# Kernel tuning notes

Measured on AMD Instinct MI355X. Metric: run time of the kernel, lower is better.

The kernel has to match this reference:

```python
import jax, jax.numpy as jnp
import numpy as np

N, K, M, DIM = 131072, 16, 128, 64


def setup_inputs() -> dict:
    key = jax.random.key(0)
    kx, ks, ka, kb = jax.random.split(key, 4)
    return {
        "x": jax.random.normal(kx, (N, DIM), dtype=jnp.float32),
        "s": jax.random.normal(ks, (K,), dtype=jnp.float32),
        "a": jax.random.normal(ka, (K, M, DIM), dtype=jnp.float32),
        "b": jax.random.normal(kb, (K, M), dtype=jnp.float32),
    }


def reference(x, s, a, b):
    # scores[k, n, m] = x[n, :] @ a[k, m, :] + b[k, m]  (batched GEMM over k)
    scores = jnp.einsum("nd,kmd->knm", x, a) + b[:, None, :]
    # per-expert logsumexp over the m affine pieces -> [k, n]
    lse = jax.nn.logsumexp(scores, axis=-1)
    # signed sum over experts -> [n]
    return jnp.einsum("k,kn->n", s, lse)
```

## Files before the change

### kernel.cpp

```cpp
#include <hip/hip_runtime.h>
#include <hip/hip_bf16.h>

#define NROWS 131072
#define KEXP 16
#define MPC 128
#define DIMD 64

typedef float f32x4  __attribute__((ext_vector_type(4)));
typedef float f32x16 __attribute__((ext_vector_type(16)));
typedef short s16x8  __attribute__((ext_vector_type(8)));

#define L2E 1.4426950408889634f
#define LN2 0.6931471805599453f

static __device__ inline unsigned int b2u(__hip_bfloat162 h) {
    union { __hip_bfloat162 h; unsigned int u; } c;
    c.h = h;
    return c.u;
}

static __device__ inline int4 cvt8s(float4 f0, float4 f1, float sc) {
    __hip_bfloat162 p0 = __float22bfloat162_rn(make_float2(f0.x * sc, f0.y * sc));
    __hip_bfloat162 p1 = __float22bfloat162_rn(make_float2(f0.z * sc, f0.w * sc));
    __hip_bfloat162 p2 = __float22bfloat162_rn(make_float2(f1.x * sc, f1.y * sc));
    __hip_bfloat162 p3 = __float22bfloat162_rn(make_float2(f1.z * sc, f1.w * sc));
    int4 pk;
    pk.x = (int)b2u(p0); pk.y = (int)b2u(p1); pk.z = (int)b2u(p2); pk.w = (int)b2u(p3);
    return pk;
}

static __device__ inline void async_copy16(const void* g, void* l) {
    __builtin_amdgcn_global_load_lds(
        (const __attribute__((address_space(1))) unsigned int*)g,
        (__attribute__((address_space(3))) unsigned int*)l, 16, 0, 0);
}

__global__ void prep_kernel(const float* __restrict__ a, const float* __restrict__ b,
                            short* __restrict__ abff) {
    const int u   = blockIdx.x * 256 + threadIdx.x;
    const int k   = u / 1280;
    const int rem = u - k * 1280;
    const int mt  = rem / 320;
    const int rc  = rem - mt * 320;
    const int c   = rc >> 6;
    const int ul  = rc & 63;
    int4 pk;
    if (c < 4) {
        const float* p = a + (size_t)(k * MPC + mt * 32 + (ul & 31)) * DIMD
                           + c * 16 + (ul >> 5) * 8;
        pk = cvt8s(*(const float4*)(p), *(const float4*)(p + 4), L2E);
    } else {
        pk.x = 0; pk.y = 0; pk.z = 0; pk.w = 0;
        if (ul < 32) {
            union { __hip_bfloat16 h; unsigned short us; } cv;
            cv.h = __float2bfloat16(b[k * MPC + mt * 32 + ul] * L2E);
            pk.x = (int)cv.us;
        }
    }
    *(int4*)(abff + (size_t)u * 8) = pk;
}

__global__ __launch_bounds__(256, 4)
void fused_kernel(const float* __restrict__ x, const float* __restrict__ s,
                  const short* __restrict__ abff, float* __restrict__ out) {
    __shared__ int4 abuf[2][1280];

    const int tid  = threadIdx.x;
    const int w    = tid >> 6;
    const int l    = tid & 63;
    const int ln   = l & 31;
    const int half = l >> 5;

    const int family = blockIdx.x & 1;
    const int r0w    = (blockIdx.x >> 1) * 256 + w * 64;

    union { int4 i; s16x8 v; } Bf[2][4];
#pragma unroll
    for (int nt = 0; nt < 2; ++nt)
#pragma unroll
        for (int c = 0; c < 4; ++c) {
            const float* gp = x + (size_t)(r0w + nt * 32 + ln) * DIMD + c * 16 + half * 8;
            float4 f0 = *(const float4*)(gp);
            float4 f1 = *(const float4*)(gp + 4);
            Bf[nt][c].i = cvt8s(f0, f1, 1.0f);
        }

    union { int4 i; s16x8 v; } Bones;
    Bones.i.x = (half == 0) ? 0x3F80 : 0;
    Bones.i.y = 0; Bones.i.z = 0; Bones.i.w = 0;

    {
        const short* src = abff + (size_t)(family * 8) * 10240;
#pragma unroll
        for (int i = 0; i < 5; ++i) {
            const int ch = w * 5 + i;
            async_copy16(src + ch * 512 + l * 8, (char*)&abuf[0][0] + ch * 1024);
        }
    }
    __syncthreads();

    float racc0 = 0.f, racc1 = 0.f;

    for (int k = 0; k < 8; ++k) {
        const int kf = family * 8 + k;
        const int kb = k & 1;

        if (k + 1 < 8) {
            const short* src = abff + (size_t)(kf + 1) * 10240;
#pragma unroll
            for (int i = 0; i < 5; ++i) {
                const int ch = w * 5 + i;
                async_copy16(src + ch * 512 + l * 8,
                             (char*)&abuf[kb ^ 1][0] + ch * 1024);
            }
        }

        const float sk2 = s[kf] * LN2;
        float esum0 = 0.f, esum1 = 0.f;

#pragma unroll
        for (int mt = 0; mt < 4; ++mt) {
            s16x8 Af[5];
#pragma unroll
            for (int c = 0; c < 5; ++c)
                Af[c] = *(const s16x8*)((const short*)&abuf[kb][0] + (mt * 5 + c) * 512 + l * 8);

            {
                f32x16 acc = {};
#pragma unroll
                for (int c = 0; c < 4; ++c)
                    acc = __builtin_amdgcn_mfma_f32_32x32x16_bf16(Af[c], Bf[0][c].v, acc, 0, 0, 0);
                acc = __builtin_amdgcn_mfma_f32_32x32x16_bf16(Af[4], Bones.v, acc, 0, 0, 0);
                float s0 = 0.f, s1 = 0.f, s2 = 0.f, s3 = 0.f;
#pragma unroll
                for (int r = 0; r < 4; ++r) {
                    s0 += __builtin_amdgcn_exp2f(acc[4 * r + 0]);
                    s1 += __builtin_amdgcn_exp2f(acc[4 * r + 1]);
                    s2 += __builtin_amdgcn_exp2f(acc[4 * r + 2]);
                    s3 += __builtin_amdgcn_exp2f(acc[4 * r + 3]);
                }
                esum0 += (s0 + s1) + (s2 + s3);
            }
            {
                f32x16 acc = {};
#pragma unroll
                for (int c = 0; c < 4; ++c)
                    acc = __builtin_amdgcn_mfma_f32_32x32x16_bf16(Af[c], Bf[1][c].v, acc, 0, 0, 0);
                acc = __builtin_amdgcn_mfma_f32_32x32x16_bf16(Af[4], Bones.v, acc, 0, 0, 0);
                float s0 = 0.f, s1 = 0.f, s2 = 0.f, s3 = 0.f;
#pragma unroll
                for (int r = 0; r < 4; ++r) {
                    s0 += __builtin_amdgcn_exp2f(acc[4 * r + 0]);
                    s1 += __builtin_amdgcn_exp2f(acc[4 * r + 1]);
                    s2 += __builtin_amdgcn_exp2f(acc[4 * r + 2]);
                    s3 += __builtin_amdgcn_exp2f(acc[4 * r + 3]);
                }
                esum1 += (s0 + s1) + (s2 + s3);
            }
        }

        float tot0 = esum0 + __shfl_xor(esum0, 32);
        float tot1 = esum1 + __shfl_xor(esum1, 32);
        racc0 = fmaf(sk2, __log2f(tot0), racc0);
        racc1 = fmaf(sk2, __log2f(tot1), racc1);

        __syncthreads();
    }

    atomicAdd(&out[r0w + half * 32 + ln], half ? racc1 : racc0);
}

extern "C" void kernel_launch(void* const* d_in, const int* in_sizes, int n_in,
                              void* d_out, int out_size, void* d_ws, size_t ws_size,
                              hipStream_t stream) {
    const float* x = (const float*)d_in[0];
    const float* s = (const float*)d_in[1];
    const float* a = (const float*)d_in[2];
    const float* b = (const float*)d_in[3];
    float* out = (float*)d_out;

    short* abff = (short*)d_ws;

    hipMemsetAsync(d_out, 0, (size_t)NROWS * sizeof(float), stream);
    prep_kernel<<<80, 256, 0, stream>>>(a, b, abff);
    fused_kernel<<<NROWS / 128, 256, 0, stream>>>(x, s, abff, out);
}
```

Measured before the change: 121.7 us.

## Split experts four ways per block, halve LDS stages, fold output zeroing into prep

Each row tile is now covered by four blocks, each handling 4 experts instead of two blocks handling 8. The grid doubles, and the per-expert weight tile is streamed in half-tiles through a smaller double-buffered LDS, which halves shared memory per block and allows 8 blocks per CU. The output memset is dropped and the zeroing moved into the prep kernel, saving one launch. The costs are that x is loaded and converted twice as often, atomics on the output double, and there are more barriers per expert.

Result: slower. 353.3 us (+190.3%).

```diff
diff --git a/kernel.cpp b/kernel.cpp
--- a/kernel.cpp
+++ b/kernel.cpp
@@ -36,7 +36,7 @@
 }
 
 __global__ void prep_kernel(const float* __restrict__ a, const float* __restrict__ b,
-                            short* __restrict__ abff) {
+                            short* __restrict__ abff, float* __restrict__ out) {
     const int u   = blockIdx.x * 256 + threadIdx.x;
     const int k   = u / 1280;
     const int rem = u - k * 1280;
@@ -58,12 +58,14 @@
         }
     }
     *(int4*)(abff + (size_t)u * 8) = pk;
-}
-
-__global__ __launch_bounds__(256, 4)
+
+    for (int i = u; i < NROWS; i += 80 * 256) out[i] = 0.f;
+}
+
+__global__ __launch_bounds__(256, 8)
 void fused_kernel(const float* __restrict__ x, const float* __restrict__ s,
                   const short* __restrict__ abff, float* __restrict__ out) {
-    __shared__ int4 abuf[2][1280];
+    __shared__ int4 abuf[2][640];
 
     const int tid  = threadIdx.x;
     const int w    = tid >> 6;
@@ -71,8 +73,8 @@
     const int ln   = l & 31;
     const int half = l >> 5;
 
-    const int family = blockIdx.x & 1;
-    const int r0w    = (blockIdx.x >> 1) * 256 + w * 64;
+    const int family = blockIdx.x & 3;
+    const int r0w    = (blockIdx.x >> 2) * 256 + w * 64;
 
     union { int4 i; s16x8 v; } Bf[2][4];
 #pragma unroll
@@ -89,82 +91,94 @@
     Bones.i.x = (half == 0) ? 0x3F80 : 0;
     Bones.i.y = 0; Bones.i.z = 0; Bones.i.w = 0;
 
+    const int kf0 = family * 4;
+
     {
-        const short* src = abff + (size_t)(family * 8) * 10240;
-#pragma unroll
-        for (int i = 0; i < 5; ++i) {
-            const int ch = w * 5 + i;
-            async_copy16(src + ch * 512 + l * 8, (char*)&abuf[0][0] + ch * 1024);
+        const short* src = abff + (size_t)kf0 * 10240;
+#pragma unroll
+        for (int i = 0; i < 3; ++i) {
+            const int ch = w + 4 * i;
+            if (ch < 10)
+                async_copy16(src + ch * 512 + l * 8, (char*)&abuf[0][0] + ch * 1024);
         }
     }
     __syncthreads();
 
     float racc0 = 0.f, racc1 = 0.f;
 
-    for (int k = 0; k < 8; ++k) {
-        const int kf = family * 8 + k;
-        const int kb = k & 1;
-
-        if (k + 1 < 8) {
-            const short* src = abff + (size_t)(kf + 1) * 10240;
-#pragma unroll
-            for (int i = 0; i < 5; ++i) {
-                const int ch = w * 5 + i;
-                async_copy16(src + ch * 512 + l * 8,
-                             (char*)&abuf[kb ^ 1][0] + ch * 1024);
-            }
-        }
-
+#pragma unroll
+    for (int k = 0; k < 4; ++k) {
+        const int kf  = kf0 + k;
         const float sk2 = s[kf] * LN2;
         float esum0 = 0.f, esum1 = 0.f;
 
 #pragma unroll
-        for (int mt = 0; mt < 4; ++mt) {
-            s16x8 Af[5];
-#pragma unroll
-            for (int c = 0; c < 5; ++c)
-                Af[c] = *(const s16x8*)((const short*)&abuf[kb][0] + (mt * 5 + c) * 512 + l * 8);
-
-            {
-                f32x16 acc = {};
-#pragma unroll
-                for (int c = 0; c < 4; ++c)
-                    acc = __builtin_amdgcn_mfma_f32_32x32x16_bf16(Af[c], Bf[0][c].v, acc, 0, 0, 0);
-                acc = __builtin_amdgcn_mfma_f32_32x32x16_bf16(Af[4], Bones.v, acc, 0, 0, 0);
-                float s0 = 0.f, s1 = 0.f, s2 = 0.f, s3 = 0.f;
-#pragma unroll
-                for (int r = 0; r < 4; ++r) {
-                    s0 += __builtin_amdgcn_exp2f(acc[4 * r + 0]);
-                    s1 += __builtin_amdgcn_exp2f(acc[4 * r + 1]);
-                    s2 += __builtin_amdgcn_exp2f(acc[4 * r + 2]);
-                    s3 += __builtin_amdgcn_exp2f(acc[4 * r + 3]);
+        for (int h = 0; h < 2; ++h) {
+            const int g   = k * 2 + h;
+            const int buf = g & 1;
+
+            if (g < 7) {
+                const int gn = g + 1;
+                const short* src = abff + (size_t)(kf0 + (gn >> 1)) * 10240
+                                        + (size_t)(gn & 1) * 5120;
+#pragma unroll
+                for (int i = 0; i < 3; ++i) {
+                    const int ch = w + 4 * i;
+                    if (ch < 10)
+                        async_copy16(src + ch * 512 + l * 8,
+                                     (char*)&abuf[buf ^ 1][0] + ch * 1024);
                 }
-                esum0 += (s0 + s1) + (s2 + s3);
             }
-            {
-                f32x16 acc = {};
-#pragma unroll
-                for (int c = 0; c < 4; ++c)
-                    acc = __builtin_amdgcn_mfma_f32_32x32x16_bf16(Af[c], Bf[1][c].v, acc, 0, 0, 0);
-                acc = __builtin_amdgcn_mfma_f32_32x32x16_bf16(Af[4], Bones.v, acc, 0, 0, 0);
-                float s0 = 0.f, s1 = 0.f, s2 = 0.f, s3 = 0.f;
-#pragma unroll
-                for (int r = 0; r < 4; ++r) {
-                    s0 += __builtin_amdgcn_exp2f(acc[4 * r + 0]);
-                    s1 += __builtin_amdgcn_exp2f(acc[4 * r + 1]);
-                    s2 += __builtin_amdgcn_exp2f(acc[4 * r + 2]);
-                    s3 += __builtin_amdgcn_exp2f(acc[4 * r + 3]);
+
+#pragma unroll
+            for (int mtl = 0; mtl < 2; ++mtl) {
+                s16x8 Af[5];
+#pragma unroll
+                for (int c = 0; c < 5; ++c)
+                    Af[c] = *(const s16x8*)((const short*)&abuf[buf][0]
+                                            + (mtl * 5 + c) * 512 + l * 8);
+
+                {
+                    f32x16 acc = {};
+#pragma unroll
+                    for (int c = 0; c < 4; ++c)
+                        acc = __builtin_amdgcn_mfma_f32_32x32x16_bf16(Af[c], Bf[0][c].v, acc, 0, 0, 0);
+                    acc = __builtin_amdgcn_mfma_f32_32x32x16_bf16(Af[4], Bones.v, acc, 0, 0, 0);
+                    float s0 = 0.f, s1 = 0.f, s2 = 0.f, s3 = 0.f;
+#pragma unroll
+                    for (int r = 0; r < 4; ++r) {
+                        s0 += __builtin_amdgcn_exp2f(acc[4 * r + 0]);
+                        s1 += __builtin_amdgcn_exp2f(acc[4 * r + 1]);
+                        s2 += __builtin_amdgcn_exp2f(acc[4 * r + 2]);
+                        s3 += __builtin_amdgcn_exp2f(acc[4 * r + 3]);
+                    }
+                    esum0 += (s0 + s1) + (s2 + s3);
                 }
-                esum1 += (s0 + s1) + (s2 + s3);
+                {
+                    f32x16 acc = {};
+#pragma unroll
+                    for (int c = 0; c < 4; ++c)
+                        acc = __builtin_amdgcn_mfma_f32_32x32x16_bf16(Af[c], Bf[1][c].v, acc, 0, 0, 0);
+                    acc = __builtin_amdgcn_mfma_f32_32x32x16_bf16(Af[4], Bones.v, acc, 0, 0, 0);
+                    float s0 = 0.f, s1 = 0.f, s2 = 0.f, s3 = 0.f;
+#pragma unroll
+                    for (int r = 0; r < 4; ++r) {
+                        s0 += __builtin_amdgcn_exp2f(acc[4 * r + 0]);
+                        s1 += __builtin_amdgcn_exp2f(acc[4 * r + 1]);
+                        s2 += __builtin_amdgcn_exp2f(acc[4 * r + 2]);
+                        s3 += __builtin_amdgcn_exp2f(acc[4 * r + 3]);
+                    }
+                    esum1 += (s0 + s1) + (s2 + s3);
+                }
             }
+
+            __syncthreads();
         }
 
         float tot0 = esum0 + __shfl_xor(esum0, 32);
         float tot1 = esum1 + __shfl_xor(esum1, 32);
         racc0 = fmaf(sk2, __log2f(tot0), racc0);
         racc1 = fmaf(sk2, __log2f(tot1), racc1);
-
-        __syncthreads();
     }
 
     atomicAdd(&out[r0w + half * 32 + ln], half ? racc1 : racc0);
@@ -181,7 +195,6 @@
 
     short* abff = (short*)d_ws;
 
-    hipMemsetAsync(d_out, 0, (size_t)NROWS * sizeof(float), stream);
-    prep_kernel<<<80, 256, 0, stream>>>(a, b, abff);
-    fused_kernel<<<NROWS / 128, 256, 0, stream>>>(x, s, abff, out);
-}
+    prep_kernel<<<80, 256, 0, stream>>>(a, b, abff, out);
+    fused_kernel<<<NROWS / 64, 256, 0, stream>>>(x, s, abff, out);
+}
```

## Fold weight conversion into main kernel and drop prep, memset and LDS staging

Applied to the files above, without the earlier changes.

Removes the separate prep kernel and output memset. Each wave now reads the fp32 expert weights straight from global memory, converts them to bf16 in registers and runs all 16 experts for 32 rows. The output is stored directly instead of added atomically. This cuts two launches, the atomics and the LDS double buffering, but every wave now repeats the global loads and bf16 conversion of a for every row tile, which adds VALU and L2 traffic inside the inner loop.

Result: slower. 302.9 us (+148.9%).

```diff
diff --git a/kernel.cpp b/kernel.cpp
--- a/kernel.cpp
+++ b/kernel.cpp
@@ -6,7 +6,6 @@
 #define MPC 128
 #define DIMD 64
 
-typedef float f32x4  __attribute__((ext_vector_type(4)));
 typedef float f32x16 __attribute__((ext_vector_type(16)));
 typedef short s16x8  __attribute__((ext_vector_type(8)));
 
@@ -29,145 +28,76 @@
     return pk;
 }
 
-static __device__ inline void async_copy16(const void* g, void* l) {
-    __builtin_amdgcn_global_load_lds(
-        (const __attribute__((address_space(1))) unsigned int*)g,
-        (__attribute__((address_space(3))) unsigned int*)l, 16, 0, 0);
-}
-
-__global__ void prep_kernel(const float* __restrict__ a, const float* __restrict__ b,
-                            short* __restrict__ abff) {
-    const int u   = blockIdx.x * 256 + threadIdx.x;
-    const int k   = u / 1280;
-    const int rem = u - k * 1280;
-    const int mt  = rem / 320;
-    const int rc  = rem - mt * 320;
-    const int c   = rc >> 6;
-    const int ul  = rc & 63;
-    int4 pk;
-    if (c < 4) {
-        const float* p = a + (size_t)(k * MPC + mt * 32 + (ul & 31)) * DIMD
-                           + c * 16 + (ul >> 5) * 8;
-        pk = cvt8s(*(const float4*)(p), *(const float4*)(p + 4), L2E);
-    } else {
-        pk.x = 0; pk.y = 0; pk.z = 0; pk.w = 0;
-        if (ul < 32) {
-            union { __hip_bfloat16 h; unsigned short us; } cv;
-            cv.h = __float2bfloat16(b[k * MPC + mt * 32 + ul] * L2E);
-            pk.x = (int)cv.us;
-        }
-    }
-    *(int4*)(abff + (size_t)u * 8) = pk;
-}
-
 __global__ __launch_bounds__(256, 4)
 void fused_kernel(const float* __restrict__ x, const float* __restrict__ s,
-                  const short* __restrict__ abff, float* __restrict__ out) {
-    __shared__ int4 abuf[2][1280];
-
+                  const float* __restrict__ a, const float* __restrict__ b,
+                  float* __restrict__ out) {
     const int tid  = threadIdx.x;
     const int w    = tid >> 6;
     const int l    = tid & 63;
     const int ln   = l & 31;
     const int half = l >> 5;
 
-    const int family = blockIdx.x & 1;
-    const int r0w    = (blockIdx.x >> 1) * 256 + w * 64;
+    const int r0 = blockIdx.x * 128 + w * 32;
 
-    union { int4 i; s16x8 v; } Bf[2][4];
+    union { int4 i; s16x8 v; } Bf[4];
 #pragma unroll
-    for (int nt = 0; nt < 2; ++nt)
-#pragma unroll
-        for (int c = 0; c < 4; ++c) {
-            const float* gp = x + (size_t)(r0w + nt * 32 + ln) * DIMD + c * 16 + half * 8;
-            float4 f0 = *(const float4*)(gp);
-            float4 f1 = *(const float4*)(gp + 4);
-            Bf[nt][c].i = cvt8s(f0, f1, 1.0f);
-        }
+    for (int c = 0; c < 4; ++c) {
+        const float* gp = x + (size_t)(r0 + ln) * DIMD + c * 16 + half * 8;
+        float4 f0 = *(const float4*)(gp);
+        float4 f1 = *(const float4*)(gp + 4);
+        Bf[c].i = cvt8s(f0, f1, 1.0f);
+    }
 
     union { int4 i; s16x8 v; } Bones;
     Bones.i.x = (half == 0) ? 0x3F80 : 0;
     Bones.i.y = 0; Bones.i.z = 0; Bones.i.w = 0;
 
-    {
-        const short* src = abff + (size_t)(family * 8) * 10240;
+    float racc = 0.f;
+
+    for (int k = 0; k < KEXP; ++k) {
+        const float* aK = a + (size_t)k * MPC * DIMD;
+        const float* bK = b + k * MPC;
+        const float sk2 = s[k] * LN2;
+
+        float s0 = 0.f, s1 = 0.f, s2 = 0.f, s3 = 0.f;
+
+        for (int mt = 0; mt < 4; ++mt) {
+            const float* ap = aK + (size_t)(mt * 32 + ln) * DIMD + half * 8;
+
+            f32x16 acc = {};
 #pragma unroll
-        for (int i = 0; i < 5; ++i) {
-            const int ch = w * 5 + i;
-            async_copy16(src + ch * 512 + l * 8, (char*)&abuf[0][0] + ch * 1024);
-        }
-    }
-    __syncthreads();
-
-    float racc0 = 0.f, racc1 = 0.f;
-
-    for (int k = 0; k < 8; ++k) {
-        const int kf = family * 8 + k;
-        const int kb = k & 1;
-
-        if (k + 1 < 8) {
-            const short* src = abff + (size_t)(kf + 1) * 10240;
+            for (int c = 0; c < 4; ++c) {
+                union { int4 i; s16x8 v; } Af;
+                float4 f0 = *(const float4*)(ap + c * 16);
+                float4 f1 = *(const float4*)(ap + c * 16 + 4);
+                Af.i = cvt8s(f0, f1, L2E);
+                acc = __builtin_amdgcn_mfma_f32_32x32x16_bf16(Af.v, Bf[c].v, acc, 0, 0, 0);
+            }
+            {
+                union { int4 i; s16x8 v; } Ab;
+                union { __hip_bfloat16 h; unsigned short us; } cb;
+                cb.h = __float2bfloat16(bK[mt * 32 + ln] * L2E);
+                Ab.i.x = (half == 0) ? (int)cb.us : 0;
+                Ab.i.y = 0; Ab.i.z = 0; Ab.i.w = 0;
+                acc = __builtin_amdgcn_mfma_f32_32x32x16_bf16(Ab.v, Bones.v, acc, 0, 0, 0);
+            }
 #pragma unroll
-            for (int i = 0; i < 5; ++i) {
-                const int ch = w * 5 + i;
-                async_copy16(src + ch * 512 + l * 8,
-                             (char*)&abuf[kb ^ 1][0] + ch * 1024);
+            for (int r = 0; r < 4; ++r) {
+                s0 += __builtin_amdgcn_exp2f(acc[4 * r + 0]);
+                s1 += __builtin_amdgcn_exp2f(acc[4 * r + 1]);
+                s2 += __builtin_amdgcn_exp2f(acc[4 * r + 2]);
+                s3 += __builtin_amdgcn_exp2f(acc[4 * r + 3]);
             }
         }
 
-        const float sk2 = s[kf] * LN2;
-        float esum0 = 0.f, esum1 = 0.f;
-
-#pragma unroll
-        for (int mt = 0; mt < 4; ++mt) {
-            s16x8 Af[5];
-#pragma unroll
-            for (int c = 0; c < 5; ++c)
-                Af[c] = *(const s16x8*)((const short*)&abuf[kb][0] + (mt * 5 + c) * 512 + l * 8);
-
-            {
-                f32x16 acc = {};
-#pragma unroll
-                for (int c = 0; c < 4; ++c)
-                    acc = __builtin_amdgcn_mfma_f32_32x32x16_bf16(Af[c], Bf[0][c].v, acc, 0, 0, 0);
-                acc = __builtin_amdgcn_mfma_f32_32x32x16_bf16(Af[4], Bones.v, acc, 0, 0, 0);
-                float s0 = 0.f, s1 = 0.f, s2 = 0.f, s3 = 0.f;
-#pragma unroll
-                for (int r = 0; r < 4; ++r) {
-                    s0 += __builtin_amdgcn_exp2f(acc[4 * r + 0]);
-                    s1 += __builtin_amdgcn_exp2f(acc[4 * r + 1]);
-                    s2 += __builtin_amdgcn_exp2f(acc[4 * r + 2]);
-                    s3 += __builtin_amdgcn_exp2f(acc[4 * r + 3]);
-                }
-                esum0 += (s0 + s1) + (s2 + s3);
-            }
-            {
-                f32x16 acc = {};
-#pragma unroll
-                for (int c = 0; c < 4; ++c)
-                    acc = __builtin_amdgcn_mfma_f32_32x32x16_bf16(Af[c], Bf[1][c].v, acc, 0, 0, 0);
-                acc = __builtin_amdgcn_mfma_f32_32x32x16_bf16(Af[4], Bones.v, acc, 0, 0, 0);
-                float s0 = 0.f, s1 = 0.f, s2 = 0.f, s3 = 0.f;
-#pragma unroll
-                for (int r = 0; r < 4; ++r) {
-                    s0 += __builtin_amdgcn_exp2f(acc[4 * r + 0]);
-                    s1 += __builtin_amdgcn_exp2f(acc[4 * r + 1]);
-                    s2 += __builtin_amdgcn_exp2f(acc[4 * r + 2]);
-                    s3 += __builtin_amdgcn_exp2f(acc[4 * r + 3]);
-                }
-                esum1 += (s0 + s1) + (s2 + s3);
-            }
-        }
-
-        float tot0 = esum0 + __shfl_xor(esum0, 32);
-        float tot1 = esum1 + __shfl_xor(esum1, 32);
-        racc0 = fmaf(sk2, __log2f(tot0), racc0);
-        racc1 = fmaf(sk2, __log2f(tot1), racc1);
-
-        __syncthreads();
+        float tot = (s0 + s1) + (s2 + s3);
+        tot += __shfl_xor(tot, 32);
+        racc = fmaf(sk2, __log2f(tot), racc);
     }
 
-    atomicAdd(&out[r0w + half * 32 + ln], half ? racc1 : racc0);
+    if (half == 0)
+        out[r0 + ln] = racc;
 }
 
 extern "C" void kernel_launch(void* const* d_in, const int* in_sizes, int n_in,
@@ -179,9 +109,5 @@
     const float* b = (const float*)d_in[3];
     float* out = (float*)d_out;
 
-    short* abff = (short*)d_ws;
-
-    hipMemsetAsync(d_out, 0, (size_t)NROWS * sizeof(float), stream);
-    prep_kernel<<<80, 256, 0, stream>>>(a, b, abff);
-    fused_kernel<<<NROWS / 128, 256, 0, stream>>>(x, s, abff, out);
+    fused_kernel<<<NROWS / 128, 256, 0, stream>>>(x, s, a, b, out);
 }
```
